# Performance work log

Hardware: AMD Instinct MI355X
Metric: run time of the kernel (lower is better)

## Reference

```python
import jax, jax.numpy as jnp
import numpy as np

A = 9          # num anchors (RPN.anchor_list)
H = W = 32     # feature-map spatial size (scaled-up from 7x7)
HID = 256      # ProposalModule hidden dim
THRESH = 0.5       # inference() thresh default
NMS_THRESH = 0.7   # inference() nms_thresh default
N = H * W * A


def _conv(x, w, b):
    y = jax.lax.conv_general_dilated(x, w, (1, 1), 'SAME',
                                     dimension_numbers=('NCHW', 'OIHW', 'NCHW'))
    return y + b[None, :, None, None]


def _pairwise_iou(boxes):
    # boxes: (N,4) [x1,y1,x2,y2]
    x1, y1, x2, y2 = boxes[:, 0], boxes[:, 1], boxes[:, 2], boxes[:, 3]
    area = jnp.maximum(x2 - x1, 0.) * jnp.maximum(y2 - y1, 0.)
    iw = jnp.maximum(jnp.minimum(x2[:, None], x2[None, :]) - jnp.maximum(x1[:, None], x1[None, :]), 0.)
    ih = jnp.maximum(jnp.minimum(y2[:, None], y2[None, :]) - jnp.maximum(y1[:, None], y1[None, :]), 0.)
    inter = iw * ih
    return inter / (area[:, None] + area[None, :] - inter + 1e-8)


def _nms_keep(boxes, scores, valid, iou_thresh):
    # greedy NMS over ALL boxes; invalid (below conf-thresh) boxes start suppressed
    n = boxes.shape[0]
    order = jnp.argsort(-scores)
    b = boxes[order]
    v = valid[order]
    iou = _pairwise_iou(b)            # (N,N) -- dominant memory traffic
    idx = jnp.arange(n)

    def body(i, sup):
        alive = jnp.logical_not(sup[i])
        return sup | (alive & (iou[i] > iou_thresh) & (idx > i))

    sup = jax.lax.fori_loop(0, n, body, jnp.logical_not(v))
    return jnp.zeros(n, bool).at[order].set(jnp.logical_not(sup))


def setup_inputs() -> dict:
    key = jax.random.key(0)
    ks = jax.random.split(key, 4)
    feat = jax.random.normal(ks[0], (1, 1280, H, W), jnp.float32)
    anchors_wh = jnp.array([[1, 1], [2, 2], [3, 3], [4, 4], [5, 5],
                            [2, 3], [3, 2], [3, 5], [5, 3]], jnp.float32)
    w1 = jax.random.normal(ks[1], (HID, 1280, 3, 3), jnp.float32) * 0.01
    b1 = jnp.zeros((HID,), jnp.float32)
    w2 = jax.random.normal(ks[2], (6 * A, HID, 1, 1), jnp.float32) * 0.05
    b2 = jax.random.normal(ks[3], (6 * A,), jnp.float32) * 0.05
    return {"feat": feat, "anchors_wh": anchors_wh, "w1": w1, "b1": b1, "w2": w2, "b2": b2}


def reference(feat, anchors_wh, w1, b1, w2, b2):
    # ProposalModule: 3x3 conv + LeakyReLU + 1x1 conv to 6A channels (dropout is identity at inference)
    h = jax.nn.leaky_relu(_conv(feat, w1, b1), 0.01)
    out = _conv(h, w2, b2)[0].reshape(A, 6, H, W)   # batch 1 -> (A,6,H,W)
    conf = jax.nn.sigmoid(out[:, 0])                 # (A,H,W), sigmoid(conf_scores[:,0])
    offs = out[:, 2:6].transpose(0, 2, 3, 1)         # (A,H,W,4) = offsets.permute(0,2,3,1)

    # GenerateGrid: cell centers at +0.5; GenerateAnchor: wh-sized boxes on each center
    xs = jnp.arange(W, dtype=feat.dtype) + 0.5
    ys = jnp.arange(H, dtype=feat.dtype) + 0.5
    cx = xs[None, None, :]
    cy = ys[None, :, None]
    aw = anchors_wh[:, 0][:, None, None]
    ah = anchors_wh[:, 1][:, None, None]

    tx, ty, tw, th = offs[..., 0], offs[..., 1], offs[..., 2], offs[..., 3]
    pcx = cx + tx * aw
    pcy = cy + ty * ah
    pw = aw * jnp.exp(tw)
    ph = ah * jnp.exp(th)
    boxes = jnp.stack([pcx - pw / 2, pcy - ph / 2, pcx + pw / 2, pcy + ph / 2], -1)  # (A,H,W,4)

    conf_f = conf.transpose(1, 2, 0).reshape(-1)          # (H*W*A,) = permute(1,2,0).reshape(-1)
    boxes_f = boxes.transpose(1, 2, 0, 3).reshape(-1, 4)  # (H*W*A,4)

    valid = conf_f > THRESH
    scores = jnp.where(valid, conf_f, -1.0)
    keep = _nms_keep(boxes_f, scores, valid, NMS_THRESH)

    k = keep.astype(boxes_f.dtype)[:, None]
    # fixed-shape masked output: kept rows are [x1,y1,x2,y2,conf], suppressed rows are 0
    return jnp.concatenate([boxes_f * k, conf_f[:, None] * k], axis=-1)  # (N,5)
```

## Files before the change

### kernel.cpp

```cpp
#include <hip/hip_runtime.h>
#include <math.h>

#define NPIX 1024
#define NBOX 9216
#define ECAP 6144

typedef unsigned long long u64;

#define O_PART     0u
#define O_H        0u
#define O_BOXES    1048576u
#define O_CONF     1196032u
#define O_KEYS     1232896u
#define O_ORDER    1306624u
#define O_SBOX     1343488u
#define O_SAREA    1490944u
#define O_EDGES    1527808u
#define O_KEEPW    1552384u
#define O_RPART    1553920u
#define O_VCNT     16777216u
#define O_ECNT     16777220u


__global__ __launch_bounds__(256, 4) void conv1_kernel(const float* __restrict__ feat,
                                                       const float* __restrict__ w1,
                                                       float* __restrict__ partial) {
    const int kc  = blockIdx.x;
    const int cog = blockIdx.y;
    const int tid = threadIdx.x;
    const int x0 = (tid & 7) * 4;
    const int y  = tid >> 3;
    const int ci0 = kc * 80;
    const int co0 = cog * 4;

    __shared__ float sf[8 * 34 * 32];

    for (int e = tid; e < 8 * 2 * 32; e += 256) {
        int ci_l = e >> 6, r = (e >> 5) & 1, c = e & 31;
        sf[(ci_l * 34 + r * 33) * 32 + c] = 0.f;
    }

    float acc[4][4];
#pragma unroll
    for (int a = 0; a < 4; ++a)
#pragma unroll
        for (int b = 0; b < 4; ++b) acc[a][b] = 0.f;

    const float* wbase = w1 + (size_t)co0 * 11520 + (size_t)ci0 * 9;

    for (int chunk = 0; chunk < 10; ++chunk) {
        const int cbase = ci0 + chunk * 8;
        __syncthreads();
        {
            const float4* fg = (const float4*)(feat + (size_t)cbase * NPIX);
#pragma unroll
            for (int k = 0; k < 8; ++k) {
                int e = tid + k * 256;
                int ci_l = e >> 8, rem = e & 255;
                int row = rem >> 3, f4c = rem & 7;
                float4 v = fg[ci_l * 256 + rem];
                *(float4*)&sf[(ci_l * 34 + row + 1) * 32 + f4c * 4] = v;
            }
        }
        __syncthreads();

#pragma unroll
        for (int cil = 0; cil < 8; ++cil) {
            float f[3][6];
            const float* base = &sf[(cil * 34 + y) * 32];
#pragma unroll
            for (int dy = 0; dy < 3; ++dy) {
                const float* rp = base + dy * 32;
                float4 mid = *(const float4*)(rp + x0);
                float lft = __int_as_float(__builtin_amdgcn_update_dpp(
                    0, __float_as_int(mid.w), 0x111 , 0xF, 0xF, true));
                float rgt = __int_as_float(__builtin_amdgcn_update_dpp(
                    0, __float_as_int(mid.x), 0x101 , 0xF, 0xF, true));
                f[dy][0] = (x0 == 0) ? 0.f : lft;
                f[dy][1] = mid.x; f[dy][2] = mid.y; f[dy][3] = mid.z; f[dy][4] = mid.w;
                f[dy][5] = (x0 == 28) ? 0.f : rgt;
            }
#pragma unroll
            for (int co = 0; co < 4; ++co) {
                const float* wrow = wbase + (size_t)co * 11520 +
                                    (size_t)(chunk * 8 + cil) * 9;
                float wv[9];
#pragma unroll
                for (int t = 0; t < 9; ++t) wv[t] = wrow[t];
#pragma unroll
                for (int dy = 0; dy < 3; ++dy)
#pragma unroll
                    for (int dx = 0; dx < 3; ++dx) {
                        float wgt = wv[dy * 3 + dx];
#pragma unroll
                        for (int px = 0; px < 4; ++px)
                            acc[co][px] = fmaf(f[dy][px + dx], wgt, acc[co][px]);
                    }
            }
        }
    }

    const int pix = y * 32 + x0;
#pragma unroll
    for (int co = 0; co < 4; ++co) {
        float4 v = {acc[co][0], acc[co][1], acc[co][2], acc[co][3]};
        *(float4*)&partial[((size_t)kc * 256 + co0 + co) * NPIX + pix] = v;
    }
}

__global__ __launch_bounds__(256) void conv1_reduce(float* part_h,
                                                    const float* __restrict__ b1) {
    int i = blockIdx.x * 256 + threadIdx.x;
    float s = b1[i >> 10];
#pragma unroll
    for (int kc = 0; kc < 16; ++kc) s += part_h[(size_t)kc * 262144 + i];
    part_h[i] = s > 0.f ? s : 0.01f * s;
}

__global__ __launch_bounds__(256) void conv2_decode(const float* __restrict__ h,
                                                    const float* __restrict__ w2,
                                                    const float* __restrict__ b2,
                                                    const float* __restrict__ anchors,
                                                    float* __restrict__ boxes,
                                                    float* __restrict__ conf_arr,
                                                    u64* __restrict__ keys,
                                                    int* __restrict__ Vcnt) {
    int gid = blockIdx.x * 256 + threadIdx.x;
    int box = gid >> 2, q = gid & 3;
    int a = box >> 10, p = box & 1023;
    const float* hq  = h + (size_t)(q * 64) * NPIX + p;
    const float* wb  = w2 + (size_t)(a * 6) * 256 + q * 64;
    float s0 = 0.f, s2 = 0.f, s3 = 0.f, s4 = 0.f, s5 = 0.f;
#pragma unroll 4
    for (int ci = 0; ci < 64; ++ci) {
        float hv = hq[(size_t)ci * NPIX];
        s0 = fmaf(hv, wb[0 * 256 + ci], s0);
        s2 = fmaf(hv, wb[2 * 256 + ci], s2);
        s3 = fmaf(hv, wb[3 * 256 + ci], s3);
        s4 = fmaf(hv, wb[4 * 256 + ci], s4);
        s5 = fmaf(hv, wb[5 * 256 + ci], s5);
    }
    s0 += __shfl_xor(s0, 1); s0 += __shfl_xor(s0, 2);
    s2 += __shfl_xor(s2, 1); s2 += __shfl_xor(s2, 2);
    s3 += __shfl_xor(s3, 1); s3 += __shfl_xor(s3, 2);
    s4 += __shfl_xor(s4, 1); s4 += __shfl_xor(s4, 2);
    s5 += __shfl_xor(s5, 1); s5 += __shfl_xor(s5, 2);
    if (q == 0) {
        s0 += b2[a * 6 + 0];
        s2 += b2[a * 6 + 2];
        s3 += b2[a * 6 + 3];
        s4 += b2[a * 6 + 4];
        s5 += b2[a * 6 + 5];
        float conf = 1.f / (1.f + expf(-s0));
        float x = (float)(p & 31), yy = (float)(p >> 5);
        float cx = x + 0.5f, cy = yy + 0.5f;
        float aw = anchors[a * 2 + 0], ah = anchors[a * 2 + 1];
        float pcx = cx + s2 * aw, pcy = cy + s3 * ah;
        float pw = aw * expf(s4), ph = ah * expf(s5);
        int idx = p * 9 + a;
        boxes[idx * 4 + 0] = pcx - pw / 2.f;
        boxes[idx * 4 + 1] = pcy - ph / 2.f;
        boxes[idx * 4 + 2] = pcx + pw / 2.f;
        boxes[idx * 4 + 3] = pcy + ph / 2.f;
        conf_arr[idx] = conf;
        bool valid = conf > 0.5f;
        float score = valid ? conf : -1.0f;
        unsigned int sb = __float_as_uint(score);
        sb = (sb & 0x80000000u) ? ~sb : (sb | 0x80000000u);
        keys[idx] = ((u64)sb << 32) | (unsigned int)(~idx);
        if (valid) atomicAdd(Vcnt, 1);
    }
}

__global__ __launch_bounds__(256) void rank_partial(const u64* __restrict__ keys,
                                                    int* __restrict__ rpart) {
    __shared__ u64 sk[256];
    int i = blockIdx.x * 256 + threadIdx.x;
    sk[threadIdx.x] = keys[blockIdx.y * 256 + threadIdx.x];
    __syncthreads();
    u64 ki = keys[i];
    int c = 0;
#pragma unroll 8
    for (int j = 0; j < 256; ++j) c += (sk[j] > ki) ? 1 : 0;
    rpart[blockIdx.y * NBOX + i] = c;
}

__global__ __launch_bounds__(256) void rank_reduce_gather(const int* __restrict__ rpart,
                                                          const float* __restrict__ boxes,
                                                          int* __restrict__ order,
                                                          float* __restrict__ sbox,
                                                          float* __restrict__ sarea) {
    int i = blockIdx.x * 256 + threadIdx.x;
    int r = 0;
    for (int b = 0; b < 36; ++b) r += rpart[b * NBOX + i];
    order[r] = i;
    float x1 = boxes[i * 4 + 0], y1 = boxes[i * 4 + 1];
    float x2 = boxes[i * 4 + 2], y2 = boxes[i * 4 + 3];
    sbox[r * 4 + 0] = x1; sbox[r * 4 + 1] = y1;
    sbox[r * 4 + 2] = x2; sbox[r * 4 + 3] = y2;
    sarea[r] = fmaxf(x2 - x1, 0.f) * fmaxf(y2 - y1, 0.f);
}

__global__ __launch_bounds__(256) void nms_edges(const float* __restrict__ sbox,
                                                 const float* __restrict__ sarea,
                                                 const int* __restrict__ Vp,
                                                 unsigned* __restrict__ edges,
                                                 int* __restrict__ Ecnt) {
    int i = blockIdx.x;
    int V = *Vp;
    if (i >= V) return;
    float x1i = sbox[i * 4 + 0], y1i = sbox[i * 4 + 1];
    float x2i = sbox[i * 4 + 2], y2i = sbox[i * 4 + 3];
    float ai = sarea[i];
    int lane = threadIdx.x & 63;
    for (int j = i + 1 + threadIdx.x; ; j += 256) {
        bool active = (j < V);
        if (__ballot(active) == 0ull) break;
        bool hit = false;
        if (active) {
            float x1j = sbox[j * 4 + 0], y1j = sbox[j * 4 + 1];
            float x2j = sbox[j * 4 + 2], y2j = sbox[j * 4 + 3];
            float iw = fmaxf(fminf(x2i, x2j) - fmaxf(x1i, x1j), 0.f);
            float ih = fmaxf(fminf(y2i, y2j) - fmaxf(y1i, y1j), 0.f);
            float inter = iw * ih;
            float iou = inter / (ai + sarea[j] - inter + 1e-8f);
            hit = iou > 0.7f;
        }
        u64 bal = __ballot(hit);
        if (bal) {
            int cnt = __popcll(bal);
            unsigned base = 0;
            if (lane == 0) base = (unsigned)atomicAdd(Ecnt, cnt);
            base = (unsigned)__shfl((int)base, 0, 64);
            if (hit) {
                int pos = (int)base + __popcll(bal & ((1ull << lane) - 1ull));
                if (pos < ECAP) edges[pos] = ((unsigned)j << 16) | (unsigned)i;
            }
        }
    }
}

__global__ __launch_bounds__(256) void nms_resolve(const unsigned* __restrict__ edges,
                                                   const int* __restrict__ Ep,
                                                   const int* __restrict__ Vp,
                                                   u64* __restrict__ keepw) {
    __shared__ unsigned se[ECAP];
    __shared__ unsigned ss[ECAP];
    __shared__ u64 sup[144];
    const int tid = threadIdx.x;
    int E = *Ep; if (E > ECAP) E = ECAP;
    const int V = *Vp;
    for (int e = tid; e < E; e += 256) se[e] = edges[e];
    for (int w = tid; w < 144; w += 256) sup[w] = 0;
    __syncthreads();
    for (int e = tid; e < E; e += 256) {
        unsigned k = se[e];
        int r = 0;
        for (int q = 0; q < E; ++q) r += (se[q] < k) ? 1 : 0;
        ss[r] = k;
    }
    __syncthreads();
    if (tid == 0) {
        for (int e = 0; e < E; ++e) {
            unsigned k = ss[e];
            int i = (int)(k & 0xffffu), j = (int)(k >> 16);
            if (!((sup[i >> 6] >> (i & 63)) & 1ull))
                sup[j >> 6] |= 1ull << (j & 63);
        }
    }
    __syncthreads();
    for (int w = tid; w < 144; w += 256) {
        int base = w * 64;
        u64 vm;
        if (base + 64 <= V) vm = ~0ull;
        else if (base >= V) vm = 0ull;
        else vm = (1ull << (V - base)) - 1ull;
        keepw[w] = ~sup[w] & vm;
    }
}

__global__ __launch_bounds__(256) void finalize(const int* __restrict__ order,
                                                const int* __restrict__ Vp,
                                                const u64* __restrict__ keepw,
                                                const float* __restrict__ boxes,
                                                const float* __restrict__ conf_arr,
                                                float* __restrict__ out) {
    int p = blockIdx.x * 256 + threadIdx.x;
    int V = *Vp;
    int o = order[p];
    bool keep = false;
    if (p < V) keep = (keepw[p >> 6] >> (p & 63)) & 1ull;
    float k = keep ? 1.f : 0.f;
    out[o * 5 + 0] = boxes[o * 4 + 0] * k;
    out[o * 5 + 1] = boxes[o * 4 + 1] * k;
    out[o * 5 + 2] = boxes[o * 4 + 2] * k;
    out[o * 5 + 3] = boxes[o * 4 + 3] * k;
    out[o * 5 + 4] = conf_arr[o] * k;
}

extern "C" void kernel_launch(void* const* d_in, const int* in_sizes, int n_in,
                              void* d_out, int out_size, void* d_ws, size_t ws_size,
                              hipStream_t stream) {
    const float* feat    = (const float*)d_in[0];
    const float* anchors = (const float*)d_in[1];
    const float* w1      = (const float*)d_in[2];
    const float* b1      = (const float*)d_in[3];
    const float* w2      = (const float*)d_in[4];
    const float* b2      = (const float*)d_in[5];
    float* out = (float*)d_out;

    char* ws = (char*)d_ws;
    float* partial = (float*)(ws + O_PART);
    float* h       = (float*)(ws + O_H);
    float* boxes   = (float*)(ws + O_BOXES);
    float* conf    = (float*)(ws + O_CONF);
    u64*   keys    = (u64*)(ws + O_KEYS);
    int* rpart     = (int*)(ws + O_RPART);
    int* order     = (int*)(ws + O_ORDER);
    float* sbox    = (float*)(ws + O_SBOX);
    float* sarea   = (float*)(ws + O_SAREA);
    int* Vcnt      = (int*)(ws + O_VCNT);
    int* Ecnt      = (int*)(ws + O_ECNT);
    u64* keepw     = (u64*)(ws + O_KEEPW);
    unsigned* edges = (unsigned*)(ws + O_EDGES);

    hipMemsetAsync(Vcnt, 0, 8, stream);

    conv1_kernel<<<dim3(16, 64), 256, 0, stream>>>(feat, w1, partial);
    conv1_reduce<<<1024, 256, 0, stream>>>(partial, b1);
    conv2_decode<<<144, 256, 0, stream>>>(h, w2, b2, anchors, boxes, conf, keys, Vcnt);
    rank_partial<<<dim3(36, 36), 256, 0, stream>>>(keys, rpart);
    rank_reduce_gather<<<36, 256, 0, stream>>>(rpart, boxes, order, sbox, sarea);
    nms_edges<<<NBOX, 256, 0, stream>>>(sbox, sarea, Vcnt, edges, Ecnt);
    nms_resolve<<<1, 256, 0, stream>>>(edges, Ecnt, Vcnt, keepw);
    finalize<<<36, 256, 0, stream>>>(order, Vcnt, keepw, boxes, conf, out);
}
```

Baseline: 226.4 us.

## Load conv tiles directly to LDS, fold memset and finalize into kernels

```diff
diff --git a/kernel.cpp b/kernel.cpp
--- a/kernel.cpp
+++ b/kernel.cpp
@@ -22,9 +22,15 @@
 #define O_ECNT     16777220u
 
 
+#define GLOAD_LDS16(g, l)                                            \
+    __builtin_amdgcn_global_load_lds(                                \
+        (const __attribute__((address_space(1))) void*)(g),          \
+        (__attribute__((address_space(3))) void*)(l), 16, 0, 0)
+
 __global__ __launch_bounds__(256, 4) void conv1_kernel(const float* __restrict__ feat,
                                                        const float* __restrict__ w1,
-                                                       float* __restrict__ partial) {
+                                                       float* __restrict__ partial,
+                                                       int* __restrict__ VE) {
     const int kc  = blockIdx.x;
     const int cog = blockIdx.y;
     const int tid = threadIdx.x;
@@ -33,6 +39,8 @@
     const int ci0 = kc * 80;
     const int co0 = cog * 4;
 
+    if (kc == 0 && cog == 0 && tid < 2) VE[tid] = 0;
+
     __shared__ float sf[8 * 34 * 32];
 
     for (int e = tid; e < 8 * 2 * 32; e += 256) {
@@ -47,6 +55,7 @@
         for (int b = 0; b < 4; ++b) acc[a][b] = 0.f;
 
     const float* wbase = w1 + (size_t)co0 * 11520 + (size_t)ci0 * 9;
+    const int wid = tid >> 6, lane = tid & 63;
 
     for (int chunk = 0; chunk < 10; ++chunk) {
         const int cbase = ci0 + chunk * 8;
@@ -54,13 +63,9 @@
         {
             const float4* fg = (const float4*)(feat + (size_t)cbase * NPIX);
 #pragma unroll
-            for (int k = 0; k < 8; ++k) {
-                int e = tid + k * 256;
-                int ci_l = e >> 8, rem = e & 255;
-                int row = rem >> 3, f4c = rem & 7;
-                float4 v = fg[ci_l * 256 + rem];
-                *(float4*)&sf[(ci_l * 34 + row + 1) * 32 + f4c * 4] = v;
-            }
+            for (int k = 0; k < 8; ++k)
+                GLOAD_LDS16(fg + k * 256 + tid,
+                            &sf[(k * 34 + 1) * 32 + wid * 256 + lane * 4]);
         }
         __syncthreads();
 
@@ -240,10 +245,13 @@
     }
 }
 
-__global__ __launch_bounds__(256) void nms_resolve(const unsigned* __restrict__ edges,
-                                                   const int* __restrict__ Ep,
-                                                   const int* __restrict__ Vp,
-                                                   u64* __restrict__ keepw) {
+__global__ __launch_bounds__(256) void nms_resolve_finalize(const unsigned* __restrict__ edges,
+                                                            const int* __restrict__ Ep,
+                                                            const int* __restrict__ Vp,
+                                                            const int* __restrict__ order,
+                                                            const float* __restrict__ boxes,
+                                                            const float* __restrict__ conf_arr,
+                                                            float* __restrict__ out) {
     __shared__ unsigned se[ECAP];
     __shared__ unsigned ss[ECAP];
     __shared__ u64 sup[144];
@@ -269,33 +277,16 @@
         }
     }
     __syncthreads();
-    for (int w = tid; w < 144; w += 256) {
-        int base = w * 64;
-        u64 vm;
-        if (base + 64 <= V) vm = ~0ull;
-        else if (base >= V) vm = 0ull;
-        else vm = (1ull << (V - base)) - 1ull;
-        keepw[w] = ~sup[w] & vm;
-    }
-}
-
-__global__ __launch_bounds__(256) void finalize(const int* __restrict__ order,
-                                                const int* __restrict__ Vp,
-                                                const u64* __restrict__ keepw,
-                                                const float* __restrict__ boxes,
-                                                const float* __restrict__ conf_arr,
-                                                float* __restrict__ out) {
-    int p = blockIdx.x * 256 + threadIdx.x;
-    int V = *Vp;
-    int o = order[p];
-    bool keep = false;
-    if (p < V) keep = (keepw[p >> 6] >> (p & 63)) & 1ull;
-    float k = keep ? 1.f : 0.f;
-    out[o * 5 + 0] = boxes[o * 4 + 0] * k;
-    out[o * 5 + 1] = boxes[o * 4 + 1] * k;
-    out[o * 5 + 2] = boxes[o * 4 + 2] * k;
-    out[o * 5 + 3] = boxes[o * 4 + 3] * k;
-    out[o * 5 + 4] = conf_arr[o] * k;
+    for (int p = tid; p < NBOX; p += 256) {
+        int o = order[p];
+        bool keep = (p < V) && !((sup[p >> 6] >> (p & 63)) & 1ull);
+        float k = keep ? 1.f : 0.f;
+        out[o * 5 + 0] = boxes[o * 4 + 0] * k;
+        out[o * 5 + 1] = boxes[o * 4 + 1] * k;
+        out[o * 5 + 2] = boxes[o * 4 + 2] * k;
+        out[o * 5 + 3] = boxes[o * 4 + 3] * k;
+        out[o * 5 + 4] = conf_arr[o] * k;
+    }
 }
 
 extern "C" void kernel_launch(void* const* d_in, const int* in_sizes, int n_in,
@@ -321,17 +312,13 @@
     float* sarea   = (float*)(ws + O_SAREA);
     int* Vcnt      = (int*)(ws + O_VCNT);
     int* Ecnt      = (int*)(ws + O_ECNT);
-    u64* keepw     = (u64*)(ws + O_KEEPW);
     unsigned* edges = (unsigned*)(ws + O_EDGES);
 
-    hipMemsetAsync(Vcnt, 0, 8, stream);
-
-    conv1_kernel<<<dim3(16, 64), 256, 0, stream>>>(feat, w1, partial);
+    conv1_kernel<<<dim3(16, 64), 256, 0, stream>>>(feat, w1, partial, Vcnt);
     conv1_reduce<<<1024, 256, 0, stream>>>(partial, b1);
     conv2_decode<<<144, 256, 0, stream>>>(h, w2, b2, anchors, boxes, conf, keys, Vcnt);
     rank_partial<<<dim3(36, 36), 256, 0, stream>>>(keys, rpart);
     rank_reduce_gather<<<36, 256, 0, stream>>>(rpart, boxes, order, sbox, sarea);
     nms_edges<<<NBOX, 256, 0, stream>>>(sbox, sarea, Vcnt, edges, Ecnt);
-    nms_resolve<<<1, 256, 0, stream>>>(edges, Ecnt, Vcnt, keepw);
-    finalize<<<36, 256, 0, stream>>>(order, Vcnt, keepw, boxes, conf, out);
-}
+    nms_resolve_finalize<<<1, 256, 0, stream>>>(edges, Ecnt, Vcnt, order, boxes, conf, out);
+}
```

After: 248.1 us. +9.6%, slower.
